# Kernel optimization log

Measured on AMD Instinct MI355X. Metric: run time of the kernel, lower is better.

The kernel has to match this reference:

```python
import jax, jax.numpy as jnp
import numpy as np


def setup_inputs() -> dict:
    key = jax.random.key(0)
    k1, k2 = jax.random.split(key)
    x = jax.random.normal(k1, (8, 64, 256, 256), dtype=jnp.float32)
    gamma = jax.random.normal(k2, (1,), dtype=jnp.float32)
    return {"x": x, "gamma": gamma}


def reference(x, gamma):
    # NOTE: the torch code does `proj_query -= avg` in-place on a view of x,
    # so proj_value (another view of x) is ALSO mean-centered. We replicate that.
    B, C, H, W = x.shape
    n = H * W
    q = x.reshape(B, C, n)
    q = q - jnp.mean(q, axis=2, keepdims=True)  # centered channels, [B,C,N]
    # energy[b,c,d] = (1/n) * sum_n q[b,c,n]*q[b,d,n]  -> [B,C,C] covariance
    energy = jnp.einsum('bcn,bdn->bcd', q, q) / n
    attention = jax.nn.softmax(energy, axis=-1)
    out = jnp.einsum('bcd,bdn->bcn', attention, q).reshape(B, C, H, W)
    return gamma * out
```

## Files before the change

kernel.cpp:

```cpp
#include <hip/hip_runtime.h>
#include <hip/hip_bf16.h>

typedef __attribute__((ext_vector_type(8))) short short8;
typedef __attribute__((ext_vector_type(4))) short short4v;
typedef __attribute__((ext_vector_type(4))) float f32x4;
typedef __attribute__((ext_vector_type(8))) __bf16 bf16x8;

#define BB 8
#define CC 64
#define NN 65536
#define SPLIT1 64
#define COLS1 (NN / SPLIT1)
#define TILE_N 256
#define SPLIT3 128

__device__ inline short f2bf(float f) {
    __hip_bfloat16 h = __float2bfloat16(f);
    return __builtin_bit_cast(short, h);
}

template <typename V>
__device__ inline auto mfma_bf16_impl(V a, V b, f32x4 c, int)
    -> decltype(__builtin_amdgcn_mfma_f32_16x16x32_bf16(a, b, c, 0, 0, 0)) {
    return __builtin_amdgcn_mfma_f32_16x16x32_bf16(a, b, c, 0, 0, 0);
}
template <typename V>
__device__ inline f32x4 mfma_bf16_impl(V a, V b, f32x4 c, long) {
    bf16x8 a2 = __builtin_bit_cast(bf16x8, a);
    bf16x8 b2 = __builtin_bit_cast(bf16x8, b);
    return __builtin_amdgcn_mfma_f32_16x16x32_bf16(a2, b2, c, 0, 0, 0);
}
__device__ inline f32x4 mfma16(short8 a, short8 b, f32x4 c) {
    return mfma_bf16_impl(a, b, c, 0);
}

__global__ __launch_bounds__(256) void k1_gram(const float* __restrict__ x,
                                               float* __restrict__ partialG,
                                               float* __restrict__ partialS) {
    __shared__ unsigned short tile[CC * TILE_N];
    const int blk  = blockIdx.x;
    const int b    = blk / SPLIT1;
    const int s    = blk % SPLIT1;
    const int tid  = threadIdx.x;
    const int w    = tid >> 6;
    const int lane = tid & 63;
    const int lg   = lane >> 4;
    const int lr   = lane & 15;

    f32x4 acc[4];
#pragma unroll
    for (int dt = 0; dt < 4; ++dt) acc[dt] = (f32x4){0.f, 0.f, 0.f, 0.f};
    float sums[16];
#pragma unroll
    for (int r = 0; r < 16; ++r) sums[r] = 0.f;

    const int colbase0 = s * COLS1;

    for (int it = 0; it < COLS1 / TILE_N; ++it) {
        const int colbase = colbase0 + it * TILE_N;
#pragma unroll
        for (int r = 0; r < 16; ++r) {
            const int row = w * 16 + r;
            const float4 v = *reinterpret_cast<const float4*>(
                x + ((size_t)(b * CC + row)) * NN + colbase + lane * 4);
            sums[r] += v.x + v.y + v.z + v.w;
            short4v sv;
            sv.x = f2bf(v.x); sv.y = f2bf(v.y); sv.z = f2bf(v.z); sv.w = f2bf(v.w);
            const int idx = ((row << 8) + lane * 4) ^ ((row & 7) << 3);
            *reinterpret_cast<short4v*>(&tile[idx]) = sv;
        }
        __syncthreads();
#pragma unroll
        for (int kk = 0; kk < TILE_N / 32; ++kk) {
            const int col = kk * 32 + lg * 8;
            const int ra  = w * 16 + lr;
            const int ia  = ((ra << 8) + col) ^ ((ra & 7) << 3);
            const short8 af = *reinterpret_cast<const short8*>(&tile[ia]);
#pragma unroll
            for (int dt = 0; dt < 4; ++dt) {
                const int rb = dt * 16 + lr;
                const int ib = ((rb << 8) + col) ^ ((rb & 7) << 3);
                const short8 bf = *reinterpret_cast<const short8*>(&tile[ib]);
                acc[dt] = mfma16(af, bf, acc[dt]);
            }
        }
        __syncthreads();
    }
#pragma unroll
    for (int dt = 0; dt < 4; ++dt) {
#pragma unroll
        for (int r = 0; r < 4; ++r) {
            const int c = w * 16 + lg * 4 + r;
            const int d = dt * 16 + lr;
            partialG[(size_t)blk * 4096 + c * 64 + d] = acc[dt][r];
        }
    }
#pragma unroll
    for (int r = 0; r < 16; ++r) {
        float v = sums[r];
        for (int off = 32; off > 0; off >>= 1) v += __shfl_down(v, off);
        if (lane == 0) partialS[blk * CC + w * 16 + r] = v;
    }
}

__global__ __launch_bounds__(256) void k2a_reduceG(const float* __restrict__ partialG,
                                                   float* __restrict__ Gsum) {
    const int gid = blockIdx.x * 256 + threadIdx.x;
    const int b = gid >> 12;
    const int e = gid & 4095;
    float s = 0.f;
    for (int sp = 0; sp < SPLIT1; ++sp)
        s += partialG[(((size_t)(b * SPLIT1 + sp)) << 12) + e];
    Gsum[gid] = s;
}

__global__ __launch_bounds__(256) void k2b_softmax(const float* __restrict__ partialS,
                                                   const float* __restrict__ Gsum,
                                                   unsigned short* __restrict__ att,
                                                   float* __restrict__ offs) {
    __shared__ float mu[CC];
    __shared__ float ener[CC * CC];
    const int b = blockIdx.x;
    const int tid = threadIdx.x;
    if (tid < CC) {
        float s = 0.f;
        for (int sp = 0; sp < SPLIT1; ++sp) s += partialS[(b * SPLIT1 + sp) * CC + tid];
        mu[tid] = s * (1.f / NN);
    }
    __syncthreads();
    const float inv_n = 1.f / NN;
#pragma unroll
    for (int k = 0; k < 16; ++k) {
        const int e = tid + k * 256;
        const int c = e >> 6, d = e & 63;
        ener[e] = Gsum[(b << 12) + e] * inv_n - mu[c] * mu[d];
    }
    __syncthreads();
    const int w = tid >> 6, lane = tid & 63;
    for (int i = 0; i < 16; ++i) {
        const int c = w * 16 + i;
        const float v = ener[c * 64 + lane];
        float m = v;
        for (int off = 32; off > 0; off >>= 1) m = fmaxf(m, __shfl_xor(m, off));
        const float ev = __expf(v - m);
        float sum = ev;
        for (int off = 32; off > 0; off >>= 1) sum += __shfl_xor(sum, off);
        const float a = ev / sum;
        att[(b << 12) + c * 64 + lane] = (unsigned short)f2bf(a);
        float o = a * mu[lane];
        for (int off = 32; off > 0; off >>= 1) o += __shfl_xor(o, off);
        if (lane == 0) offs[b * CC + c] = o;
    }
}

__global__ __launch_bounds__(256) void k3_apply(const float* __restrict__ x,
                                                const unsigned short* __restrict__ att,
                                                const float* __restrict__ offs,
                                                const float* __restrict__ gamma,
                                                float* __restrict__ out) {
    const int blk  = blockIdx.x;
    const int b    = blk / SPLIT3;
    const int s    = blk % SPLIT3;
    const int tid  = threadIdx.x;
    const int w    = tid >> 6, lane = tid & 63, lg = lane >> 4, lr = lane & 15;
    const float g  = gamma[0];

    short8 afr[4][2];
#pragma unroll
    for (int ct = 0; ct < 4; ++ct)
#pragma unroll
        for (int ks = 0; ks < 2; ++ks)
            afr[ct][ks] = *reinterpret_cast<const short8*>(
                att + (((size_t)b) << 12) + (ct * 16 + lr) * 64 + ks * 32 + lg * 8);

    float offv[4][4];
#pragma unroll
    for (int ct = 0; ct < 4; ++ct)
#pragma unroll
        for (int r = 0; r < 4; ++r)
            offv[ct][r] = offs[b * CC + ct * 16 + lg * 4 + r];

    const int colblock = s * (NN / SPLIT3);
    const int GROUPS = (NN / SPLIT3) / (4 * 64);
    for (int itg = 0; itg < GROUPS; ++itg) {
        const int n0 = colblock + (w * GROUPS + itg) * 64;
        f32x4 acc[4][4];
#pragma unroll
        for (int ph = 0; ph < 4; ++ph)
#pragma unroll
            for (int ct = 0; ct < 4; ++ct) acc[ph][ct] = (f32x4){0.f, 0.f, 0.f, 0.f};

#pragma unroll
        for (int ks = 0; ks < 2; ++ks) {
            short8 bfr[4];
            const int d0 = ks * 32 + lg * 8;
            const float* xp = x + ((size_t)(b * CC + d0)) * NN + n0 + lr * 4;
#pragma unroll
            for (int j = 0; j < 8; ++j) {
                const float4 v = *reinterpret_cast<const float4*>(xp + (size_t)j * NN);
                bfr[0][j] = f2bf(v.x);
                bfr[1][j] = f2bf(v.y);
                bfr[2][j] = f2bf(v.z);
                bfr[3][j] = f2bf(v.w);
            }
#pragma unroll
            for (int ct = 0; ct < 4; ++ct) {
#pragma unroll
                for (int ph = 0; ph < 4; ++ph)
                    acc[ph][ct] = mfma16(afr[ct][ks], bfr[ph], acc[ph][ct]);
            }
        }
#pragma unroll
        for (int ct = 0; ct < 4; ++ct) {
#pragma unroll
            for (int r = 0; r < 4; ++r) {
                const int c = ct * 16 + lg * 4 + r;
                const float o = offv[ct][r];
                f32x4 vs;
                vs[0] = g * (acc[0][ct][r] - o);
                vs[1] = g * (acc[1][ct][r] - o);
                vs[2] = g * (acc[2][ct][r] - o);
                vs[3] = g * (acc[3][ct][r] - o);
                __builtin_nontemporal_store(
                    vs, reinterpret_cast<f32x4*>(out + ((size_t)(b * CC + c)) * NN + n0 + lr * 4));
            }
        }
    }
}

extern "C" void kernel_launch(void* const* d_in, const int* in_sizes, int n_in,
                              void* d_out, int out_size, void* d_ws, size_t ws_size,
                              hipStream_t stream) {
    const float* x     = (const float*)d_in[0];
    const float* gamma = (const float*)d_in[1];
    float* out = (float*)d_out;

    float* partialG = out;
    float* partialS = out + (size_t)BB * SPLIT1 * 4096;
    float* Gsum     = partialS + BB * SPLIT1 * CC;
    float* offs     = (float*)d_ws;
    unsigned short* att = (unsigned short*)((char*)d_ws + 4096);

    k1_gram<<<BB * SPLIT1, 256, 0, stream>>>(x, partialG, partialS);
    k2a_reduceG<<<(BB * 4096) / 256, 256, 0, stream>>>(partialG, Gsum);
    k2b_softmax<<<BB, 256, 0, stream>>>(partialS, Gsum, att, offs);
    k3_apply<<<BB * SPLIT3, 256, 0, stream>>>(x, att, offs, gamma, out);
}
```

Baseline: 93.05 us.

## Double-buffer Gram tiles with register prefetch and fuse G reduction into softmax

The Gram kernel now prefetches the next column tile into registers while MFMAs run on the current LDS buffer, using two LDS buffers and a single barrier per iteration. This is meant to hide global load latency. The separate partial-Gram reduction kernel is folded into the softmax kernel, which saves a launch and the Gsum round trip. The trade-off is that only 8 blocks now reduce 64 partial tiles each, which serialises that reduction onto very few CUs, and the extra registers and LDS may lower occupancy.

```diff
diff --git a/kernel.cpp b/kernel.cpp
--- a/kernel.cpp
+++ b/kernel.cpp
@@ -12,6 +12,7 @@
 #define SPLIT1 64
 #define COLS1 (NN / SPLIT1)
 #define TILE_N 256
+#define NT1 (COLS1 / TILE_N)
 #define SPLIT3 128
 
 __device__ inline short f2bf(float f) {
@@ -34,10 +35,10 @@
     return mfma_bf16_impl(a, b, c, 0);
 }
 
-__global__ __launch_bounds__(256) void k1_gram(const float* __restrict__ x,
-                                               float* __restrict__ partialG,
-                                               float* __restrict__ partialS) {
-    __shared__ unsigned short tile[CC * TILE_N];
+__global__ __launch_bounds__(256, 2) void k1_gram(const float* __restrict__ x,
+                                                  float* __restrict__ partialG,
+                                                  float* __restrict__ partialS) {
+    __shared__ unsigned short tile[2][CC * TILE_N];
     const int blk  = blockIdx.x;
     const int b    = blk / SPLIT1;
     const int s    = blk % SPLIT1;
@@ -55,33 +56,57 @@
     for (int r = 0; r < 16; ++r) sums[r] = 0.f;
 
     const int colbase0 = s * COLS1;
-
-    for (int it = 0; it < COLS1 / TILE_N; ++it) {
-        const int colbase = colbase0 + it * TILE_N;
-#pragma unroll
-        for (int r = 0; r < 16; ++r) {
-            const int row = w * 16 + r;
-            const float4 v = *reinterpret_cast<const float4*>(
-                x + ((size_t)(b * CC + row)) * NN + colbase + lane * 4);
-            sums[r] += v.x + v.y + v.z + v.w;
-            short4v sv;
-            sv.x = f2bf(v.x); sv.y = f2bf(v.y); sv.z = f2bf(v.z); sv.w = f2bf(v.w);
-            const int idx = ((row << 8) + lane * 4) ^ ((row & 7) << 3);
-            *reinterpret_cast<short4v*>(&tile[idx]) = sv;
-        }
-        __syncthreads();
+    float4 pf[16];
+
+#pragma unroll
+    for (int r = 0; r < 16; ++r)
+        pf[r] = *reinterpret_cast<const float4*>(
+            x + ((size_t)(b * CC + w * 16 + r)) * NN + colbase0 + lane * 4);
+#pragma unroll
+    for (int r = 0; r < 16; ++r) {
+        const int row = w * 16 + r;
+        const float4 v = pf[r];
+        sums[r] += v.x + v.y + v.z + v.w;
+        short4v sv;
+        sv.x = f2bf(v.x); sv.y = f2bf(v.y); sv.z = f2bf(v.z); sv.w = f2bf(v.w);
+        const int idx = ((row << 8) + lane * 4) ^ ((row & 7) << 3);
+        *reinterpret_cast<short4v*>(&tile[0][idx]) = sv;
+    }
+    __syncthreads();
+
+    for (int it = 0; it < NT1; ++it) {
+        const int cur = it & 1;
+        if (it + 1 < NT1) {
+            const int colbase = colbase0 + (it + 1) * TILE_N;
+#pragma unroll
+            for (int r = 0; r < 16; ++r)
+                pf[r] = *reinterpret_cast<const float4*>(
+                    x + ((size_t)(b * CC + w * 16 + r)) * NN + colbase + lane * 4);
+        }
 #pragma unroll
         for (int kk = 0; kk < TILE_N / 32; ++kk) {
             const int col = kk * 32 + lg * 8;
             const int ra  = w * 16 + lr;
             const int ia  = ((ra << 8) + col) ^ ((ra & 7) << 3);
-            const short8 af = *reinterpret_cast<const short8*>(&tile[ia]);
+            const short8 af = *reinterpret_cast<const short8*>(&tile[cur][ia]);
 #pragma unroll
             for (int dt = 0; dt < 4; ++dt) {
                 const int rb = dt * 16 + lr;
                 const int ib = ((rb << 8) + col) ^ ((rb & 7) << 3);
-                const short8 bf = *reinterpret_cast<const short8*>(&tile[ib]);
+                const short8 bf = *reinterpret_cast<const short8*>(&tile[cur][ib]);
                 acc[dt] = mfma16(af, bf, acc[dt]);
+            }
+        }
+        if (it + 1 < NT1) {
+#pragma unroll
+            for (int r = 0; r < 16; ++r) {
+                const int row = w * 16 + r;
+                const float4 v = pf[r];
+                sums[r] += v.x + v.y + v.z + v.w;
+                short4v sv;
+                sv.x = f2bf(v.x); sv.y = f2bf(v.y); sv.z = f2bf(v.z); sv.w = f2bf(v.w);
+                const int idx = ((row << 8) + lane * 4) ^ ((row & 7) << 3);
+                *reinterpret_cast<short4v*>(&tile[cur ^ 1][idx]) = sv;
             }
         }
         __syncthreads();
@@ -103,43 +128,42 @@
     }
 }
 
-__global__ __launch_bounds__(256) void k2a_reduceG(const float* __restrict__ partialG,
-                                                   float* __restrict__ Gsum) {
-    const int gid = blockIdx.x * 256 + threadIdx.x;
-    const int b = gid >> 12;
-    const int e = gid & 4095;
-    float s = 0.f;
-    for (int sp = 0; sp < SPLIT1; ++sp)
-        s += partialG[(((size_t)(b * SPLIT1 + sp)) << 12) + e];
-    Gsum[gid] = s;
-}
-
-__global__ __launch_bounds__(256) void k2b_softmax(const float* __restrict__ partialS,
-                                                   const float* __restrict__ Gsum,
-                                                   unsigned short* __restrict__ att,
-                                                   float* __restrict__ offs) {
+__global__ __launch_bounds__(256) void k2_fused(const float* __restrict__ partialG,
+                                                const float* __restrict__ partialS,
+                                                unsigned short* __restrict__ att,
+                                                float* __restrict__ offs) {
     __shared__ float mu[CC];
     __shared__ float ener[CC * CC];
     const int b = blockIdx.x;
     const int tid = threadIdx.x;
+
     if (tid < CC) {
         float s = 0.f;
         for (int sp = 0; sp < SPLIT1; ++sp) s += partialS[(b * SPLIT1 + sp) * CC + tid];
         mu[tid] = s * (1.f / NN);
     }
+    f32x4 sg[4];
+#pragma unroll
+    for (int p = 0; p < 4; ++p) sg[p] = (f32x4){0.f, 0.f, 0.f, 0.f};
+    for (int sp = 0; sp < SPLIT1; ++sp) {
+        const f32x4* base = reinterpret_cast<const f32x4*>(
+            partialG + (((size_t)(b * SPLIT1 + sp)) << 12));
+#pragma unroll
+        for (int p = 0; p < 4; ++p) sg[p] += base[tid + p * 256];
+    }
+    const float inv_n = 1.f / NN;
+#pragma unroll
+    for (int p = 0; p < 4; ++p) {
+        f32x4 v = sg[p];
+        v[0] *= inv_n; v[1] *= inv_n; v[2] *= inv_n; v[3] *= inv_n;
+        *reinterpret_cast<f32x4*>(&ener[(tid + p * 256) * 4]) = v;
+    }
     __syncthreads();
-    const float inv_n = 1.f / NN;
-#pragma unroll
-    for (int k = 0; k < 16; ++k) {
-        const int e = tid + k * 256;
-        const int c = e >> 6, d = e & 63;
-        ener[e] = Gsum[(b << 12) + e] * inv_n - mu[c] * mu[d];
-    }
-    __syncthreads();
+
     const int w = tid >> 6, lane = tid & 63;
     for (int i = 0; i < 16; ++i) {
         const int c = w * 16 + i;
-        const float v = ener[c * 64 + lane];
+        const float v = ener[c * 64 + lane] - mu[c] * mu[lane];
         float m = v;
         for (int off = 32; off > 0; off >>= 1) m = fmaxf(m, __shfl_xor(m, off));
         const float ev = __expf(v - m);
@@ -237,12 +261,10 @@
 
     float* partialG = out;
     float* partialS = out + (size_t)BB * SPLIT1 * 4096;
-    float* Gsum     = partialS + BB * SPLIT1 * CC;
     float* offs     = (float*)d_ws;
     unsigned short* att = (unsigned short*)((char*)d_ws + 4096);
 
     k1_gram<<<BB * SPLIT1, 256, 0, stream>>>(x, partialG, partialS);
-    k2a_reduceG<<<(BB * 4096) / 256, 256, 0, stream>>>(partialG, Gsum);
-    k2b_softmax<<<BB, 256, 0, stream>>>(partialS, Gsum, att, offs);
+    k2_fused<<<BB, 256, 0, stream>>>(partialG, partialS, att, offs);
     k3_apply<<<BB * SPLIT3, 256, 0, stream>>>(x, att, offs, gamma, out);
 }
```

New measurement: 126.8 us. +36.3%, slower.

## Double-buffer Gram kernel with async global-to-LDS fp32 staging

Applied to the files above, without the earlier changes.

The Gram kernel now copies fp32 tiles straight from global memory into a double-buffered, swizzled LDS area using global_load_lds, so the next tile's load overlaps MFMA work on the current one. The bf16 conversion and the row-sum accumulation move to after the LDS read and happen inside the MFMA loop. The B operand is converted redundantly in every wave, which adds VALU work and doubles the LDS footprint and traffic because the tile is stored as fp32. The per-row sum reduction becomes a two-step xor shuffle.

```diff
diff --git a/kernel.cpp b/kernel.cpp
--- a/kernel.cpp
+++ b/kernel.cpp
@@ -11,7 +11,8 @@
 #define NN 65536
 #define SPLIT1 64
 #define COLS1 (NN / SPLIT1)
-#define TILE_N 256
+#define TILE_C 128
+#define NT1 (COLS1 / TILE_C)
 #define SPLIT3 128
 
 __device__ inline short f2bf(float f) {
@@ -34,53 +35,79 @@
     return mfma_bf16_impl(a, b, c, 0);
 }
 
+__device__ inline void stage_tile(const float* __restrict__ xb, int colbase,
+                                  float* buf, int tid) {
+    const int half = tid >> 5;
+    const int sl   = tid & 31;
+#pragma unroll
+    for (int i = 0; i < 8; ++i) {
+        const int row   = i * 8 + half;
+        const int gbyte = (sl * 16) ^ ((row & 31) << 4);
+        const float* gp = xb + (size_t)row * NN + colbase + (gbyte >> 2);
+        float* lp = buf + i * 1024 + tid * 4;
+#if __has_builtin(__builtin_amdgcn_global_load_lds)
+        __builtin_amdgcn_global_load_lds(
+            (const __attribute__((address_space(1))) void*)gp,
+            (__attribute__((address_space(3))) void*)lp, 16, 0, 0);
+#else
+        *reinterpret_cast<f32x4*>(lp) = *reinterpret_cast<const f32x4*>(gp);
+#endif
+    }
+}
+
+__device__ inline void lds_read8(const float* buf, int row, int c0, float* v) {
+    const char* rb = (const char*)(buf + row * TILE_C);
+    const int swz = (row & 31) << 4;
+    const f32x4 u0 = *reinterpret_cast<const f32x4*>(rb + ((c0 * 4) ^ swz));
+    const f32x4 u1 = *reinterpret_cast<const f32x4*>(rb + (((c0 * 4) + 16) ^ swz));
+    v[0] = u0[0]; v[1] = u0[1]; v[2] = u0[2]; v[3] = u0[3];
+    v[4] = u1[0]; v[5] = u1[1]; v[6] = u1[2]; v[7] = u1[3];
+}
+
+__device__ inline short8 cvt8(const float* v) {
+    short8 r;
+#pragma unroll
+    for (int j = 0; j < 8; ++j) r[j] = f2bf(v[j]);
+    return r;
+}
+
 __global__ __launch_bounds__(256) void k1_gram(const float* __restrict__ x,
                                                float* __restrict__ partialG,
                                                float* __restrict__ partialS) {
-    __shared__ unsigned short tile[CC * TILE_N];
+    __shared__ float lbuf[2][CC * TILE_C];
     const int blk  = blockIdx.x;
     const int b    = blk / SPLIT1;
     const int s    = blk % SPLIT1;
     const int tid  = threadIdx.x;
-    const int w    = tid >> 6;
-    const int lane = tid & 63;
-    const int lg   = lane >> 4;
-    const int lr   = lane & 15;
+    const int w    = tid >> 6, lane = tid & 63, lg = lane >> 4, lr = lane & 15;
+    const float* xb = x + (size_t)b * CC * NN;
+    const int colbase0 = s * COLS1;
 
     f32x4 acc[4];
 #pragma unroll
     for (int dt = 0; dt < 4; ++dt) acc[dt] = (f32x4){0.f, 0.f, 0.f, 0.f};
-    float sums[16];
-#pragma unroll
-    for (int r = 0; r < 16; ++r) sums[r] = 0.f;
-
-    const int colbase0 = s * COLS1;
-
-    for (int it = 0; it < COLS1 / TILE_N; ++it) {
-        const int colbase = colbase0 + it * TILE_N;
-#pragma unroll
-        for (int r = 0; r < 16; ++r) {
-            const int row = w * 16 + r;
-            const float4 v = *reinterpret_cast<const float4*>(
-                x + ((size_t)(b * CC + row)) * NN + colbase + lane * 4);
-            sums[r] += v.x + v.y + v.z + v.w;
-            short4v sv;
-            sv.x = f2bf(v.x); sv.y = f2bf(v.y); sv.z = f2bf(v.z); sv.w = f2bf(v.w);
-            const int idx = ((row << 8) + lane * 4) ^ ((row & 7) << 3);
-            *reinterpret_cast<short4v*>(&tile[idx]) = sv;
-        }
-        __syncthreads();
-#pragma unroll
-        for (int kk = 0; kk < TILE_N / 32; ++kk) {
-            const int col = kk * 32 + lg * 8;
-            const int ra  = w * 16 + lr;
-            const int ia  = ((ra << 8) + col) ^ ((ra & 7) << 3);
-            const short8 af = *reinterpret_cast<const short8*>(&tile[ia]);
+    float asum = 0.f;
+
+    stage_tile(xb, colbase0, lbuf[0], tid);
+    __syncthreads();
+
+    for (int t = 0; t < NT1; ++t) {
+        if (t + 1 < NT1)
+            stage_tile(xb, colbase0 + (t + 1) * TILE_C, lbuf[(t + 1) & 1], tid);
+        const float* buf = lbuf[t & 1];
+#pragma unroll
+        for (int kk = 0; kk < TILE_C / 32; ++kk) {
+            const int c0 = kk * 32 + lg * 8;
+            float av[8];
+            lds_read8(buf, w * 16 + lr, c0, av);
+#pragma unroll
+            for (int j = 0; j < 8; ++j) asum += av[j];
+            const short8 af = cvt8(av);
 #pragma unroll
             for (int dt = 0; dt < 4; ++dt) {
-                const int rb = dt * 16 + lr;
-                const int ib = ((rb << 8) + col) ^ ((rb & 7) << 3);
-                const short8 bf = *reinterpret_cast<const short8*>(&tile[ib]);
+                float bv[8];
+                lds_read8(buf, dt * 16 + lr, c0, bv);
+                const short8 bf = cvt8(bv);
                 acc[dt] = mfma16(af, bf, acc[dt]);
             }
         }
@@ -95,12 +122,10 @@
             partialG[(size_t)blk * 4096 + c * 64 + d] = acc[dt][r];
         }
     }
-#pragma unroll
-    for (int r = 0; r < 16; ++r) {
-        float v = sums[r];
-        for (int off = 32; off > 0; off >>= 1) v += __shfl_down(v, off);
-        if (lane == 0) partialS[blk * CC + w * 16 + r] = v;
-    }
+    float v = asum;
+    v += __shfl_xor(v, 16);
+    v += __shfl_xor(v, 32);
+    if (lg == 0) partialS[blk * CC + w * 16 + lr] = v;
 }
 
 __global__ __launch_bounds__(256) void k2a_reduceG(const float* __restrict__ partialG,
```

Measured after the change: 84.24 us. 9.5% less time.
